# Performance work log

Measured on AMD Instinct MI355X. Metric: run time of the kernel, lower is better.

Reference implementation:

```python
import jax, jax.numpy as jnp
import numpy as np

N_CLASSES = 40
EMBED_DIM = 128
MOMENTUM = 0.1
LAMBDA_R, LAMBDA_C, LAMBDA_M = 1.0, 0.5, 1.0
BATCH = 262144


def setup_inputs() -> dict:
    key = jax.random.key(0)
    k1, k2, k3 = jax.random.split(key, 3)
    z = jax.random.normal(k1, (BATCH, EMBED_DIM), dtype=jnp.float32)
    y = jax.random.randint(k2, (BATCH,), 0, N_CLASSES)
    centers = jax.random.normal(k3, (N_CLASSES, EMBED_DIM), dtype=jnp.float32)
    initialized = jnp.ones((N_CLASSES,), dtype=bool)
    # buffers derived from class_counts (imbalanced ramp), r0=gamma=m0=1, alpha=0.25
    counts = jnp.asarray([1000.0 * (i + 1) for i in range(N_CLASSES)], jnp.float32)
    n_max = jnp.max(counts)
    target_radii = 1.0 + 1.0 * jnp.log(n_max / (counts + 1.0))
    margins = 1.0 * jnp.power(n_max / (counts + 1.0), 0.25)
    return {"z": z, "y": y, "centers": centers, "initialized": initialized,
            "target_radii": target_radii, "margins": margins}


def _update_centers(z, y, centers, initialized):
    # EMA centroid update on detached embeddings (torch.no_grad equivalent).
    zs = jax.lax.stop_gradient(z)
    sums = jax.ops.segment_sum(zs, y, num_segments=N_CLASSES)            # [C, D]
    cnt = jax.ops.segment_sum(jnp.ones((zs.shape[0],), zs.dtype), y,
                              num_segments=N_CLASSES)                    # [C]
    mean = sums / jnp.maximum(cnt, 1.0)[:, None]
    ema = (1.0 - MOMENTUM) * centers + MOMENTUM * mean
    new = jnp.where(initialized[:, None], ema, mean)                     # first-touch init
    return jnp.where((cnt > 0)[:, None], new, centers)                   # skip empty classes


def reference(z, y, centers, initialized, target_radii, margins):
    c = _update_centers(z, y, centers, initialized)                      # [C, D]

    # radial loss: smooth L1 (beta=1) between ||z|| and per-class target radius
    r = jnp.linalg.norm(z, axis=-1)                                      # [B]
    d = r - target_radii[y]
    ad = jnp.abs(d)
    loss_radial = jnp.mean(jnp.where(ad < 1.0, 0.5 * d * d, ad - 0.5))

    # compact loss: mean squared distance to own centroid
    diff = z - c[y]                                                      # [B, D]
    loss_compact = jnp.mean(jnp.sum(diff * diff, axis=-1))

    # margin loss: min distance to any other class centroid via Gram trick
    z2 = jnp.sum(z * z, axis=-1)                                         # [B]
    c2 = jnp.sum(c * c, axis=-1)                                         # [C]
    d2 = z2[:, None] + c2[None, :] - 2.0 * (z @ c.T)                     # [B, C]
    dist = jnp.sqrt(jnp.maximum(d2, 0.0))
    own = y[:, None] == jnp.arange(N_CLASSES)[None, :]                   # [B, C] bool
    dist_opp = jnp.min(jnp.where(own, jnp.inf, dist), axis=1)            # [B]
    loss_margin = jnp.mean(jax.nn.relu(margins[y] - dist_opp))

    return LAMBDA_R * loss_radial + LAMBDA_C * loss_compact + LAMBDA_M * loss_margin
```

## Files before the change

kernel.cpp:

```cpp
#include <hip/hip_runtime.h>
#include <math.h>

#define BATCH 262144
#define DIM   128
#define NCLS  40
#define NCP   48
#define CD    (NCLS * DIM)

#define TB1 256
#define NB1 256
#define TB3 256
#define NB3 (BATCH / 256)

typedef __attribute__((ext_vector_type(8))) short short8;
typedef __attribute__((ext_vector_type(4))) float f32x4;

__device__ __forceinline__ short f2bf(float f) {
    unsigned u = __float_as_uint(f);
    u += 0x7fffu + ((u >> 16) & 1u);
    return (short)(u >> 16);
}

__global__ __launch_bounds__(TB1) void k1_segsum(const float* __restrict__ z,
                                                 const int* __restrict__ y,
                                                 float* __restrict__ ps,
                                                 float* __restrict__ gcnt) {
    __shared__ float s_acc[4][NCLS * DIM];
    __shared__ float s_cnt[NCLS];

    const int t    = threadIdx.x;
    const int w    = t >> 6;
    const int lane = t & 63;

    {
        float4* az = (float4*)&s_acc[0][0];
        const float4 z4 = make_float4(0.f, 0.f, 0.f, 0.f);
        for (int i = t; i < 4 * NCLS * DIM / 4; i += TB1) az[i] = z4;
        if (t < NCLS) s_cnt[t] = 0.0f;
    }
    __syncthreads();

    const int rbase = blockIdx.x * 1024 + w * 256;

    const int2 yA = ((const int2*)(y + rbase))[lane];
    const int2 yB = ((const int2*)(y + rbase + 128))[lane];
    atomicAdd(&s_cnt[yA.x], 1.0f);
    atomicAdd(&s_cnt[yA.y], 1.0f);
    atomicAdd(&s_cnt[yB.x], 1.0f);
    atomicAdd(&s_cnt[yB.y], 1.0f);

    const float* __restrict__ zw = z + (size_t)rbase * DIM;
    float* __restrict__ accw = s_acc[w];

    float4 vb[8];
#pragma unroll
    for (int q = 0; q < 8; ++q)
        vb[q] = *(const float4*)(zw + (size_t)q * 256 + lane * 4);

#define K1_HALF(YH, GB, CLAMP)                                                \
    _Pragma("unroll 1")                                                       \
    for (int i0 = 0; i0 < 64; i0 += 8) {                                      \
        _Pragma("unroll")                                                     \
        for (int q = 0; q < 8; ++q) {                                         \
            const int i2 = i0 + q;                                            \
            float4 v = vb[q];                                                 \
            int g = (GB) + i2 + 8;                                            \
            if (CLAMP && g > 127) g = (GB) + i2;    \
            vb[q] = *(const float4*)(zw + (size_t)g * 256 + lane * 4);        \
            const int c0 = __builtin_amdgcn_readlane((YH).x, i2);             \
            const int c1 = __builtin_amdgcn_readlane((YH).y, i2);             \
            if (c0 != c1) {       \
                const int cls = (lane < 32) ? c0 : c1;                        \
                float4* ap = (float4*)&accw[cls * DIM] + (lane & 31);         \
                float4 o = *ap;                                               \
                o.x += v.x; o.y += v.y; o.z += v.z; o.w += v.w;               \
                *ap = o;                                                      \
            } else {           \
                v.x += __shfl_xor(v.x, 32);                                   \
                v.y += __shfl_xor(v.y, 32);                                   \
                v.z += __shfl_xor(v.z, 32);                                   \
                v.w += __shfl_xor(v.w, 32);                                   \
                if (lane < 32) {                                              \
                    float4* ap = (float4*)&accw[c0 * DIM] + lane;             \
                    float4 o = *ap;                                           \
                    o.x += v.x; o.y += v.y; o.z += v.z; o.w += v.w;           \
                    *ap = o;                                                  \
                }                                                             \
            }                                                                 \
        }                                                                     \
    }

    K1_HALF(yA, 0, 0)
    K1_HALF(yB, 64, 1)
#undef K1_HALF

    __syncthreads();

    float4* __restrict__ psb = (float4*)(ps + (size_t)blockIdx.x * CD);
    const float4* a0 = (const float4*)s_acc[0];
    const float4* a1 = (const float4*)s_acc[1];
    const float4* a2 = (const float4*)s_acc[2];
    const float4* a3 = (const float4*)s_acc[3];
#pragma unroll
    for (int k = 0; k < 5; ++k) {
        const int j = t + k * TB1;
        const float4 p0 = a0[j], p1 = a1[j], p2 = a2[j], p3 = a3[j];
        float4 r;
        r.x = (p0.x + p1.x) + (p2.x + p3.x);
        r.y = (p0.y + p1.y) + (p2.y + p3.y);
        r.z = (p0.z + p1.z) + (p2.z + p3.z);
        r.w = (p0.w + p1.w) + (p2.w + p3.w);
        psb[j] = r;
    }
    if (t < NCLS) atomicAdd(&gcnt[t], s_cnt[t]);
}

__global__ __launch_bounds__(512) void k2_centers(const float* __restrict__ ps,
                                                  const float* __restrict__ gcnt,
                                                  const float* __restrict__ centers,
                                                  short* __restrict__ cbf,
                                                  float* __restrict__ c2p) {
    const int j    = blockIdx.x >> 1;
    const int half = blockIdx.x & 1;
    const int t    = threadIdx.x;
    const int dl   = t & 63;
    const int d    = half * 64 + dl;
    const int s    = t >> 6;

    if (j >= NCLS) {
        if (s == 0) cbf[j * DIM + d] = 0;
        if (t == 0) c2p[blockIdx.x] = 5e29f;
        return;
    }

    const float* __restrict__ p = ps + j * DIM + d + (size_t)(s * 32) * CD;
    float sum = 0.0f;
#pragma unroll 8
    for (int b = 0; b < 32; ++b) sum += p[(size_t)b * CD];

    __shared__ float red[512];
    red[t] = sum;
    __syncthreads();

    if (s == 0) {
        float tot = 0.0f;
#pragma unroll
        for (int k = 0; k < 8; ++k) tot += red[(k << 6) | dl];
        const float cnt  = gcnt[j];
        const float mean = tot / fmaxf(cnt, 1.0f);
        const float ctr  = centers[j * DIM + d];
        const float ema  = 0.9f * ctr + 0.1f * mean;
        const float cv   = (cnt > 0.0f) ? ema : ctr;
        cbf[j * DIM + d] = f2bf(cv);
        red[t] = cv * cv;
    }
    __syncthreads();
    if (t == 0) {
        float sc = 0.0f;
#pragma unroll 8
        for (int i = 0; i < 64; ++i) sc += red[i];
        c2p[blockIdx.x] = sc;
    }
}

__global__ __launch_bounds__(TB3) void k3_loss(const float* __restrict__ z,
                                               const int* __restrict__ y,
                                               const short* __restrict__ cbf,
                                               const float* __restrict__ c2p,
                                               const float* __restrict__ tr,
                                               const float* __restrict__ mg,
                                               float* __restrict__ out) {
    __shared__ float s_S[4][64 * 52];
    __shared__ float s_c2[NCP];

    const int t = threadIdx.x;
    if (t < NCP) s_c2[t] = c2p[2 * t] + c2p[2 * t + 1];

    const int w    = t >> 6;
    const int lane = t & 63;
    const int q    = lane >> 4;
    const int col  = lane & 15;
    const int wavebase = blockIdx.x * 256 + w * 64;

    short8 bfrag[3][4];
#pragma unroll
    for (int ct = 0; ct < 3; ++ct)
#pragma unroll
        for (int s = 0; s < 4; ++s)
            bfrag[ct][s] = *(const short8*)(cbf + (ct * 16 + col) * DIM + s * 32 + q * 8);

    __syncthreads();

#pragma unroll 1
    for (int rt = 0; rt < 4; ++rt) {
        const float* __restrict__ zrow =
            z + (size_t)(wavebase + rt * 16 + col) * DIM + q * 8;

        float4 f[8];
#pragma unroll
        for (int s = 0; s < 4; ++s) {
            f[2 * s]     = *(const float4*)(zrow + s * 32);
            f[2 * s + 1] = *(const float4*)(zrow + s * 32 + 4);
        }

        float zp = 0.0f;
#pragma unroll
        for (int i = 0; i < 8; ++i) {
            zp = fmaf(f[i].x, f[i].x, zp);
            zp = fmaf(f[i].y, f[i].y, zp);
            zp = fmaf(f[i].z, f[i].z, zp);
            zp = fmaf(f[i].w, f[i].w, zp);
        }

        short8 afr[4];
#pragma unroll
        for (int s = 0; s < 4; ++s) {
            const float4 f0 = f[2 * s], f1 = f[2 * s + 1];
            afr[s][0] = f2bf(f0.x); afr[s][1] = f2bf(f0.y);
            afr[s][2] = f2bf(f0.z); afr[s][3] = f2bf(f0.w);
            afr[s][4] = f2bf(f1.x); afr[s][5] = f2bf(f1.y);
            afr[s][6] = f2bf(f1.z); afr[s][7] = f2bf(f1.w);
        }

        f32x4 acc0 = {0.f, 0.f, 0.f, 0.f};
        f32x4 acc1 = {0.f, 0.f, 0.f, 0.f};
        f32x4 acc2 = {0.f, 0.f, 0.f, 0.f};
#pragma unroll
        for (int s = 0; s < 4; ++s) {
            acc0 = __builtin_amdgcn_mfma_f32_16x16x32_bf16(afr[s], bfrag[0][s], acc0, 0, 0, 0);
            acc1 = __builtin_amdgcn_mfma_f32_16x16x32_bf16(afr[s], bfrag[1][s], acc1, 0, 0, 0);
            acc2 = __builtin_amdgcn_mfma_f32_16x16x32_bf16(afr[s], bfrag[2][s], acc2, 0, 0, 0);
        }

        zp += __shfl_xor(zp, 16);
        zp += __shfl_xor(zp, 32);
        if (q == 0) s_S[w][(rt * 16 + col) * 52 + 48] = zp;

#pragma unroll
        for (int reg = 0; reg < 4; ++reg) {
            const int rr = rt * 16 + q * 4 + reg;
            s_S[w][rr * 52 + col]      = acc0[reg];
            s_S[w][rr * 52 + 16 + col] = acc1[reg];
            s_S[w][rr * 52 + 32 + col] = acc2[reg];
        }
    }

    const int row = blockIdx.x * 256 + t;
    const int cls = y[row];
    const float z2v = s_S[w][lane * 52 + 48];

    float own_d2 = 0.0f;
    float mind2  = 3.4e38f;
#pragma unroll
    for (int k = 0; k < 12; ++k) {
        const float4 Sv = *(const float4*)&s_S[w][lane * 52 + 4 * k];
        const float Se[4] = {Sv.x, Sv.y, Sv.z, Sv.w};
#pragma unroll
        for (int e = 0; e < 4; ++e) {
            const int j = 4 * k + e;
            float d2 = fmaxf(z2v + s_c2[j] - 2.0f * Se[e], 0.0f);
            const bool isown = (j == cls);
            own_d2 = isown ? d2 : own_d2;
            mind2  = isown ? mind2 : fminf(mind2, d2);
        }
    }

    const float r  = sqrtf(z2v);
    const float dd = r - tr[cls];
    const float ad = fabsf(dd);
    const float rad = (ad < 1.0f) ? 0.5f * dd * dd : ad - 0.5f;

    const float dist = sqrtf(mind2);
    const float marg = fmaxf(mg[cls] - dist, 0.0f);

    const float tot = rad + 0.5f * own_d2 + marg;

    __syncthreads();
    float* s_red = &s_S[0][0];
    s_red[t] = tot;
    __syncthreads();
    for (int off = TB3 / 2; off > 0; off >>= 1) {
        if (t < off) s_red[t] += s_red[t + off];
        __syncthreads();
    }
    if (t == 0) atomicAdd(out, s_red[0] * (1.0f / (float)BATCH));
}

extern "C" void kernel_launch(void* const* d_in, const int* in_sizes, int n_in,
                              void* d_out, int out_size, void* d_ws, size_t ws_size,
                              hipStream_t stream) {
    const float* z       = (const float*)d_in[0];
    const int*   y       = (const int*)d_in[1];
    const float* centers = (const float*)d_in[2];
    const float* tr      = (const float*)d_in[4];
    const float* mg      = (const float*)d_in[5];
    float* out = (float*)d_out;

    float* ws        = (float*)d_ws;
    float* part_sums = ws;
    float* c2p       = part_sums + (size_t)NB1 * CD;
    float* gcnt      = c2p + 2 * NCP;
    short* cbf       = (short*)(gcnt + NCLS);

    hipMemsetAsync(gcnt, 0, NCLS * sizeof(float), stream);
    hipMemsetAsync(out, 0, sizeof(float), stream);

    k1_segsum<<<NB1, TB1, 0, stream>>>(z, y, part_sums, gcnt);
    k2_centers<<<2 * NCP, 512, 0, stream>>>(part_sums, gcnt, centers, cbf, c2p);
    k3_loss<<<NB3, TB3, 0, stream>>>(z, y, cbf, c2p, tr, mg, out);
}
```

Measured before the change: 240.2 us.

## Stream segment-sum rows through LDS ring via async global_load_lds, drop memsets

The segment-sum kernel now streams rows of z directly into a per-wave 8-slot LDS ring using async global-to-LDS loads with explicit vmcnt waits, instead of holding a register prefetch buffer. It also changes the row-to-lane mapping so each wave reads labels once via int2. Global count atomics and the two memsets are replaced by per-block partial counts that the centers kernel reduces, and that kernel also zeroes the output. This is meant to cut register pressure and launch overhead, at the cost of extra LDS and hand-tuned wait counts.

```diff
diff --git a/kernel.cpp b/kernel.cpp
--- a/kernel.cpp
+++ b/kernel.cpp
@@ -21,10 +21,17 @@
     return (short)(u >> 16);
 }
 
+__device__ __forceinline__ void k1_stage(const float* src, float* dst) {
+    __builtin_amdgcn_global_load_lds(
+        (const __attribute__((address_space(1))) void*)src,
+        (__attribute__((address_space(3))) void*)dst, 16, 0, 0);
+}
+
 __global__ __launch_bounds__(TB1) void k1_segsum(const float* __restrict__ z,
                                                  const int* __restrict__ y,
                                                  float* __restrict__ ps,
-                                                 float* __restrict__ gcnt) {
+                                                 float* __restrict__ part_cnt) {
+    __shared__ float s_ring[4][8 * 256];
     __shared__ float s_acc[4][NCLS * DIM];
     __shared__ float s_cnt[NCLS];
 
@@ -42,57 +49,60 @@
 
     const int rbase = blockIdx.x * 1024 + w * 256;
 
-    const int2 yA = ((const int2*)(y + rbase))[lane];
-    const int2 yB = ((const int2*)(y + rbase + 128))[lane];
-    atomicAdd(&s_cnt[yA.x], 1.0f);
-    atomicAdd(&s_cnt[yA.y], 1.0f);
-    atomicAdd(&s_cnt[yB.x], 1.0f);
-    atomicAdd(&s_cnt[yB.y], 1.0f);
-
-    const float* __restrict__ zw = z + (size_t)rbase * DIM;
-    float* __restrict__ accw = s_acc[w];
-
-    float4 vb[8];
-#pragma unroll
-    for (int q = 0; q < 8; ++q)
-        vb[q] = *(const float4*)(zw + (size_t)q * 256 + lane * 4);
-
-#define K1_HALF(YH, GB, CLAMP)                                                \
-    _Pragma("unroll 1")                                                       \
-    for (int i0 = 0; i0 < 64; i0 += 8) {                                      \
-        _Pragma("unroll")                                                     \
-        for (int q = 0; q < 8; ++q) {                                         \
-            const int i2 = i0 + q;                                            \
-            float4 v = vb[q];                                                 \
-            int g = (GB) + i2 + 8;                                            \
-            if (CLAMP && g > 127) g = (GB) + i2;    \
-            vb[q] = *(const float4*)(zw + (size_t)g * 256 + lane * 4);        \
-            const int c0 = __builtin_amdgcn_readlane((YH).x, i2);             \
-            const int c1 = __builtin_amdgcn_readlane((YH).y, i2);             \
-            if (c0 != c1) {       \
-                const int cls = (lane < 32) ? c0 : c1;                        \
-                float4* ap = (float4*)&accw[cls * DIM] + (lane & 31);         \
+    const int2 y2 = ((const int2*)(y + rbase))[lane];
+    atomicAdd(&s_cnt[y2.x], 1.0f);
+    atomicAdd(&s_cnt[y2.y], 1.0f);
+
+    const float* __restrict__ zw   = z + (size_t)rbase * DIM;
+    float* __restrict__ ringw      = s_ring[w];
+    float* __restrict__ accw       = s_acc[w];
+
+#pragma unroll
+    for (int p = 0; p < 8; ++p)
+        k1_stage(zw + (size_t)p * 256 + lane * 4, ringw + p * 256);
+
+#define K1_BODY(P)                                                            \
+    {                                                                         \
+        const int slot = (P) & 7;                                             \
+        float4 v = *(const float4*)(ringw + slot * 256 + lane * 4);           \
+        const int c0 = __builtin_amdgcn_readlane(y2.x, (P));                  \
+        const int c1 = __builtin_amdgcn_readlane(y2.y, (P));                  \
+        if (c0 != c1) {     \
+            const int cls = (lane < 32) ? c0 : c1;                            \
+            float4* ap = (float4*)&accw[cls * DIM] + (lane & 31);             \
+            float4 o = *ap;                                                   \
+            o.x += v.x; o.y += v.y; o.z += v.z; o.w += v.w;                   \
+            *ap = o;                                                          \
+        } else {               \
+            v.x += __shfl_xor(v.x, 32);                                       \
+            v.y += __shfl_xor(v.y, 32);                                       \
+            v.z += __shfl_xor(v.z, 32);                                       \
+            v.w += __shfl_xor(v.w, 32);                                       \
+            if (lane < 32) {                                                  \
+                float4* ap = (float4*)&accw[c0 * DIM] + lane;                 \
                 float4 o = *ap;                                               \
                 o.x += v.x; o.y += v.y; o.z += v.z; o.w += v.w;               \
                 *ap = o;                                                      \
-            } else {           \
-                v.x += __shfl_xor(v.x, 32);                                   \
-                v.y += __shfl_xor(v.y, 32);                                   \
-                v.z += __shfl_xor(v.z, 32);                                   \
-                v.w += __shfl_xor(v.w, 32);                                   \
-                if (lane < 32) {                                              \
-                    float4* ap = (float4*)&accw[c0 * DIM] + lane;             \
-                    float4 o = *ap;                                           \
-                    o.x += v.x; o.y += v.y; o.z += v.z; o.w += v.w;           \
-                    *ap = o;                                                  \
-                }                                                             \
             }                                                                 \
         }                                                                     \
     }
 
-    K1_HALF(yA, 0, 0)
-    K1_HALF(yB, 64, 1)
-#undef K1_HALF
+#pragma unroll 1
+    for (int p = 0; p < 120; ++p) {
+        asm volatile("s_waitcnt vmcnt(7)" ::: "memory");
+        __builtin_amdgcn_sched_barrier(0);
+        K1_BODY(p)
+        k1_stage(zw + (size_t)(p + 8) * 256 + lane * 4, ringw + (p & 7) * 256);
+    }
+
+#define K1_TAIL(P, W)                                                         \
+    asm volatile("s_waitcnt vmcnt(" #W ")" ::: "memory");                     \
+    __builtin_amdgcn_sched_barrier(0);                                        \
+    K1_BODY(P)
+    K1_TAIL(120, 7) K1_TAIL(121, 6) K1_TAIL(122, 5) K1_TAIL(123, 4)
+    K1_TAIL(124, 3) K1_TAIL(125, 2) K1_TAIL(126, 1) K1_TAIL(127, 0)
+#undef K1_TAIL
+#undef K1_BODY
 
     __syncthreads();
 
@@ -112,14 +122,15 @@
         r.w = (p0.w + p1.w) + (p2.w + p3.w);
         psb[j] = r;
     }
-    if (t < NCLS) atomicAdd(&gcnt[t], s_cnt[t]);
+    if (t < NCLS) part_cnt[blockIdx.x * NCLS + t] = s_cnt[t];
 }
 
 __global__ __launch_bounds__(512) void k2_centers(const float* __restrict__ ps,
-                                                  const float* __restrict__ gcnt,
+                                                  const float* __restrict__ part_cnt,
                                                   const float* __restrict__ centers,
                                                   short* __restrict__ cbf,
-                                                  float* __restrict__ c2p) {
+                                                  float* __restrict__ c2p,
+                                                  float* __restrict__ out) {
     const int j    = blockIdx.x >> 1;
     const int half = blockIdx.x & 1;
     const int t    = threadIdx.x;
@@ -127,6 +138,8 @@
     const int d    = half * 64 + dl;
     const int s    = t >> 6;
 
+    if (blockIdx.x == 0 && t == 0) out[0] = 0.0f;
+
     if (j >= NCLS) {
         if (s == 0) cbf[j * DIM + d] = 0;
         if (t == 0) c2p[blockIdx.x] = 5e29f;
@@ -146,7 +159,14 @@
         float tot = 0.0f;
 #pragma unroll
         for (int k = 0; k < 8; ++k) tot += red[(k << 6) | dl];
-        const float cnt  = gcnt[j];
+
+        float cpart = 0.0f;
+#pragma unroll
+        for (int i = 0; i < 4; ++i) cpart += part_cnt[(dl * 4 + i) * NCLS + j];
+#pragma unroll
+        for (int off = 1; off < 64; off <<= 1) cpart += __shfl_xor(cpart, off);
+        const float cnt = cpart;
+
         const float mean = tot / fmaxf(cnt, 1.0f);
         const float ctr  = centers[j * DIM + d];
         const float ema  = 0.9f * ctr + 0.1f * mean;
@@ -298,14 +318,12 @@
 
     float* ws        = (float*)d_ws;
     float* part_sums = ws;
-    float* c2p       = part_sums + (size_t)NB1 * CD;
-    float* gcnt      = c2p + 2 * NCP;
-    short* cbf       = (short*)(gcnt + NCLS);
-
-    hipMemsetAsync(gcnt, 0, NCLS * sizeof(float), stream);
-    hipMemsetAsync(out, 0, sizeof(float), stream);
-
-    k1_segsum<<<NB1, TB1, 0, stream>>>(z, y, part_sums, gcnt);
-    k2_centers<<<2 * NCP, 512, 0, stream>>>(part_sums, gcnt, centers, cbf, c2p);
+    float* part_cnt  = part_sums + (size_t)NB1 * CD;
+    float* c2p       = part_cnt + (size_t)NB1 * NCLS;
+    short* cbf       = (short*)(c2p + 2 * NCP);
+
+    k1_segsum<<<NB1, TB1, 0, stream>>>(z, y, part_sums, part_cnt);
+    k2_centers<<<2 * NCP, 512, 0, stream>>>(part_sums, part_cnt, centers, cbf,
+                                            c2p, out);
     k3_loss<<<NB3, TB3, 0, stream>>>(z, y, cbf, c2p, tr, mg, out);
 }
```

Result: slower. 279.4 us (+16.3%).
